# Optimization experiments

Hardware: AMD Instinct MI355X
Metric: run time of the kernel (lower is better)

## Reference

```python
import jax, jax.numpy as jnp
import numpy as np
import math

B, H, W, C = 8, 32, 32, 512
NUM_HEAD_CHANNELS = 64
NUM_HEADS = C // NUM_HEAD_CHANNELS  # 8
HEAD_DIM = C // NUM_HEADS            # 64
NUM_GROUPS = max(1, C // 16)         # 32
EPS = 1e-6  # flax GroupNorm default epsilon


def setup_inputs() -> dict:
    key = jax.random.key(0)
    ks = jax.random.split(key, 7)
    s = lambda fan: 1.0 / math.sqrt(fan)
    return {
        "x": jax.random.normal(ks[0], (B, H, W, C), jnp.float32),
        "gn_scale": jnp.ones((C,), jnp.float32),
        "gn_bias": jnp.zeros((C,), jnp.float32),
        "w_qkv": jax.random.normal(ks[1], (C, 3 * C), jnp.float32) * s(C),
        "b_qkv": jnp.zeros((3 * C,), jnp.float32),
        "w_out": jax.random.normal(ks[2], (C, C), jnp.float32) * s(C),
        "b_out": jnp.zeros((C,), jnp.float32),
    }


def _group_norm(x, scale, bias):
    # x: (B,H,W,C); normalize per (batch, group) over spatial + in-group channels
    b, h, w, c = x.shape
    xg = x.reshape(b, h * w, NUM_GROUPS, c // NUM_GROUPS)
    mu = jnp.mean(xg, axis=(1, 3), keepdims=True)
    var = jnp.var(xg, axis=(1, 3), keepdims=True)
    xn = (xg - mu) * jax.lax.rsqrt(var + EPS)
    return xn.reshape(b, h, w, c) * scale + bias


def reference(x, gn_scale, gn_bias, w_qkv, b_qkv, w_out, b_out):
    b, h, w, c = x.shape
    seq = h * w
    x_flat = x.reshape(b, seq, c)
    x_norm = _group_norm(x, gn_scale, gn_bias).reshape(b, seq, c)
    qkv = x_norm @ w_qkv + b_qkv                      # (b, seq, 3c)
    q, k, v = jnp.split(qkv, 3, axis=-1)
    scale = 1.0 / math.sqrt(HEAD_DIM)

    def to_heads(t):
        return t.reshape(b, seq, NUM_HEADS, HEAD_DIM).transpose(0, 2, 1, 3)

    q, k, v = to_heads(q), to_heads(k), to_heads(v)
    # NOTE: scale applied to both q and k, matching the original module
    weight = jnp.einsum('bhld,bhsd->bhls', q * scale, k * scale)
    weight = jax.nn.softmax(weight, axis=-1)
    out = jnp.einsum('bhls,bhsd->bhld', weight, v)
    out = out.transpose(0, 2, 1, 3).reshape(b, seq, c)
    out = out @ w_out + b_out
    return (x_flat + out).reshape(b, h, w, c)
```

## Files before the change

### kernel.cpp

```cpp
#include <hip/hip_runtime.h>
#include <hip/hip_bf16.h>

#define SEQ   1024
#define CH    512
#define NHEAD 8
#define HDIM  64
#define BATCH 8

using short8  = __attribute__((ext_vector_type(8))) short;
using short4v = __attribute__((ext_vector_type(4))) short;
using floatx4 = __attribute__((ext_vector_type(4))) float;
using uint4v  = __attribute__((ext_vector_type(4))) unsigned int;

#if __has_builtin(__builtin_amdgcn_exp2f)
#define EXP2F __builtin_amdgcn_exp2f
#else
#define EXP2F exp2f
#endif

__device__ inline unsigned short f2bf(float f) {
  __hip_bfloat16 h = __float2bfloat16(f);
  return __builtin_bit_cast(unsigned short, h);
}

__device__ inline unsigned int cvt_pk_bf16(float lo, float hi) {
  unsigned int r;
  asm("v_cvt_pk_bf16_f32 %0, %1, %2" : "=v"(r) : "v"(lo), "v"(hi));
  return r;
}

__device__ inline void load_lds16(const void* g, void* l) {
  __builtin_amdgcn_global_load_lds(
      (const __attribute__((address_space(1))) unsigned int*)g,
      (__attribute__((address_space(3))) unsigned int*)l, 16, 0, 0);
}

__global__ __launch_bounds__(1024) void prep_kernel(
    const float* __restrict__ wqkv, const float* __restrict__ wout,
    const float* __restrict__ x, const float* __restrict__ gsc,
    const float* __restrict__ gbs,
    unsigned short* __restrict__ wqkvt, unsigned short* __restrict__ woutt,
    unsigned short* __restrict__ xn) {
  __shared__ float SH[16416];
  const int blk = blockIdx.x, tid = threadIdx.x;

  if (blk >= 256) {
    const float* src; unsigned short* dst; int C, bx, by;
    if (blk < 448) { int t = blk - 256; src = wqkv; dst = wqkvt; C = 1536; bx = t % 24; by = t / 24; }
    else           { int t = blk - 448; src = wout; dst = woutt; C = 512;  bx = t & 7;  by = t >> 3; }
    float (*T)[65] = (float(*)[65])SH;
    int tx = tid & 63, ty = tid >> 6;
    for (int j = 0; j < 4; ++j)
      T[ty + j * 16][tx] = src[(size_t)(by * 64 + ty + j * 16) * C + bx * 64 + tx];
    __syncthreads();
    for (int j = 0; j < 4; ++j)
      dst[(size_t)(bx * 64 + ty + j * 16) * 512 + by * 64 + tx] = f2bf(T[tx][ty + j * 16]);
    return;
  }

  const int b = blk >> 5, g = blk & 31;
  const size_t base = (size_t)b * SEQ * CH + g * 16;

  float s = 0.f, sq = 0.f;
  for (int i = 0; i < 4; ++i) {
    int c = (i << 10) + tid;
    int r = c >> 2, c4 = (c & 3) << 2;
    float4 v = *(const float4*)(x + base + (size_t)r * CH + c4);
    *(float4*)&SH[c << 2] = v;
    s  += v.x + v.y + v.z + v.w;
    sq += v.x * v.x + v.y * v.y + v.z * v.z + v.w * v.w;
  }
  for (int off = 1; off < 64; off <<= 1) {
    s  += __shfl_xor(s, off);
    sq += __shfl_xor(sq, off);
  }
  const int wid = tid >> 6, lane = tid & 63;
  if (lane == 0) { SH[16384 + wid] = s; SH[16400 + wid] = sq; }
  __syncthreads();
  float ts = 0.f, tq = 0.f;
  for (int i = 0; i < 16; ++i) { ts += SH[16384 + i]; tq += SH[16400 + i]; }
  const float inv_n = 1.0f / 16384.0f;
  float mean = ts * inv_n;
  float var  = tq * inv_n - mean * mean;
  float rstd = rsqrtf(var + 1e-6f);

  int c4 = (tid & 3) << 2;
  float4 sc = *(const float4*)(gsc + g * 16 + c4);
  float4 bs = *(const float4*)(gbs + g * 16 + c4);
  for (int i = 0; i < 4; ++i) {
    int c = (i << 10) + tid;
    int r = c >> 2;
    float4 v = *(const float4*)&SH[c << 2];
    ushort4 o;
    o.x = f2bf((v.x - mean) * rstd * sc.x + bs.x);
    o.y = f2bf((v.y - mean) * rstd * sc.y + bs.y);
    o.z = f2bf((v.z - mean) * rstd * sc.z + bs.z);
    o.w = f2bf((v.w - mean) * rstd * sc.w + bs.w);
    *(ushort4*)(xn + base + (size_t)r * CH + c4) = o;
  }
}

template <int EPI, int MTILE>
__global__ __launch_bounds__(256) void gemm_bt_kernel(
    const unsigned short* __restrict__ A, const unsigned short* __restrict__ Bt,
    int K, int N,
    const float* __restrict__ bias, const float* __restrict__ resid,
    float* __restrict__ outf,
    unsigned short* __restrict__ qb, unsigned short* __restrict__ kb,
    unsigned short* __restrict__ vtb) {
  constexpr int SMSZ = (MTILE == 128) ? 17408 : 16896;
  constexpr int NI   = (MTILE == 128) ? 4 : 2;
  __shared__ alignas(16) unsigned short SM[SMSZ];
  unsigned short* LA = SM;
  unsigned short* LB = SM + MTILE * 64;

  const int tid = threadIdx.x;
  const int wid = tid >> 6, lane = tid & 63;
  const int quad = lane >> 4, m16 = lane & 15;
  const int sw = m16 & 7;
  const int wm = (MTILE == 128) ? (wid & 1) * 64 : 0;
  const int wn = (MTILE == 128) ? (wid >> 1) * 64 : wid * 32;
  const int m0 = blockIdx.x * MTILE, n0 = blockIdx.y * 128;

  floatx4 acc[4][NI];
  for (int i = 0; i < 4; ++i)
    for (int j = 0; j < NI; ++j) acc[i][j] = 0.f;

  for (int k0 = 0; k0 < K; k0 += 64) {
    for (int i = 0; i < MTILE / 32; ++i) {
      int c = i * 256 + tid;
      int r = c >> 3, kc = c & 7;
      load_lds16(A + (size_t)(m0 + r) * K + k0 + ((kc ^ (r & 7)) << 3), &LA[c << 3]);
    }
    for (int i = 0; i < 4; ++i) {
      int c = i * 256 + tid;
      int r = c >> 3, kc = c & 7;
      load_lds16(Bt + (size_t)(n0 + r) * K + k0 + ((kc ^ (r & 7)) << 3), &LB[c << 3]);
    }
    __syncthreads();
    for (int kq = 0; kq < 2; ++kq) {
      int csw = (((kq << 2) + quad) ^ sw) << 3;
      short8 af[4], bf[NI];
      for (int mi = 0; mi < 4; ++mi)
        af[mi] = *(const short8*)&LA[(wm + mi * 16 + m16) * 64 + csw];
      for (int ni = 0; ni < NI; ++ni)
        bf[ni] = *(const short8*)&LB[(wn + ni * 16 + m16) * 64 + csw];
      for (int mi = 0; mi < 4; ++mi)
        for (int ni = 0; ni < NI; ++ni)
          acc[mi][ni] = __builtin_amdgcn_mfma_f32_16x16x32_bf16(af[mi], bf[ni], acc[mi][ni], 0, 0, 0);
    }
    __syncthreads();
  }

  const int b = m0 >> 10;
  if (EPI == 0) {
    const int part = n0 >> 9;
    if (part < 2) {
      const float qscale = (part == 0) ? 0.0225421381f : 1.0f;
      unsigned short* dst = (part == 0) ? qb : kb;
      for (int mi = 0; mi < 4; ++mi)
        for (int ni = 0; ni < 4; ++ni) {
          int ln = wn + ni * 16 + m16;
          float bb = bias[n0 + ln];
          for (int reg = 0; reg < 4; ++reg)
            SM[(wm + mi * 16 + quad * 4 + reg) * 136 + ln] =
                f2bf((acc[mi][ni][reg] + bb) * qscale);
        }
      __syncthreads();
      const int colb = n0 & 511;
      for (int j = 0; j < 8; ++j) {
        int c = j * 256 + tid;
        int m = c >> 4, n8 = (c & 15) * 8;
        int h = (colb + n8) >> 6, d = n8 & 63;
        int sp = (m0 & 1023) + m;
        int4 v = *(const int4*)&SM[m * 136 + n8];
        *(int4*)(dst + (((size_t)(b * NHEAD + h)) * SEQ + sp) * HDIM + d) = v;
      }
    } else {
      for (int mi = 0; mi < 4; ++mi)
        for (int ni = 0; ni < 4; ++ni) {
          int ln = wn + ni * 16 + m16;
          float bb = bias[n0 + ln];
          int mblk = (wm >> 4) + mi;
          int sbase = 32 * (mblk >> 1) + 8 * quad + 4 * (mblk & 1);
          for (int reg = 0; reg < 4; ++reg)
            SM[ln * 136 + sbase + reg] = f2bf(acc[mi][ni][reg] + bb);
        }
      __syncthreads();
      int hbase = (n0 - 1024) >> 6;
      for (int j = 0; j < 8; ++j) {
        int c = j * 256 + tid;
        int ld = c >> 4, sp8 = (c & 15) * 8;
        int h = hbase + (ld >> 6), d = ld & 63;
        int4 v = *(const int4*)&SM[ld * 136 + sp8];
        *(int4*)(vtb + ((size_t)(b * NHEAD + h) * HDIM + d) * SEQ + (m0 & 1023) + sp8) = v;
      }
    }
  } else {
    float* SMf = (float*)SM;
    for (int mi = 0; mi < 4; ++mi)
      for (int ni = 0; ni < NI; ++ni) {
        int ln = wn + ni * 16 + m16;
        float bb = bias[n0 + ln];
        for (int reg = 0; reg < 4; ++reg)
          SMf[(mi * 16 + quad * 4 + reg) * 132 + ln] = acc[mi][ni][reg] + bb;
      }
    __syncthreads();
    for (int j = 0; j < 8; ++j) {
      int c = j * 256 + tid;
      int m = c >> 5, n4 = (c & 31) * 4;
      size_t idx = (size_t)(m0 + m) * N + n0 + n4;
      float4 v = *(const float4*)&SMf[m * 132 + n4];
      float4 rr = *(const float4*)&resid[idx];
      v.x += rr.x; v.y += rr.y; v.z += rr.z; v.w += rr.w;
      *(float4*)&outf[idx] = v;
    }
  }
}

__global__ __launch_bounds__(256) void attn_kernel(
    const unsigned short* __restrict__ qb, const unsigned short* __restrict__ kb,
    const unsigned short* __restrict__ vtb, unsigned short* __restrict__ ao) {
  const int head = blockIdx.x, qt = blockIdx.y;
  const int b = head >> 3, h = head & 7;
  const int tid = threadIdx.x;
  const int wid = tid >> 6, lane = tid & 63;
  const int quad = lane >> 4, m16 = lane & 15;
  const int sw = m16 & 7;

  __shared__ alignas(16) unsigned short sK[2][8192];
  __shared__ alignas(16) unsigned short sV[2][8192];

  const unsigned short* kbase = kb  + (size_t)head * SEQ * HDIM;
  const unsigned short* vbase = vtb + (size_t)head * HDIM * SEQ;

  short8 aq[2][2];
  for (int qblk = 0; qblk < 2; ++qblk) {
    const size_t qrow = (size_t)head * SEQ + qt * 128 + wid * 32 + qblk * 16 + m16;
    aq[qblk][0] = *(const short8*)(qb + qrow * HDIM + quad * 8);
    aq[qblk][1] = *(const short8*)(qb + qrow * HDIM + 32 + quad * 8);
  }

  const unsigned int onep = 0x3F803F80u;
  const short8 vones = __builtin_bit_cast(short8, (uint4v){onep, onep, onep, onep});

  floatx4 la[2];
  floatx4 o[2][4];
  for (int qblk = 0; qblk < 2; ++qblk) {
    la[qblk] = 0.f;
    for (int df = 0; df < 4; ++df) o[qblk][df] = 0.f;
  }

  for (int i = 0; i < 4; ++i) {
    int c = i * 256 + tid;
    int r = c >> 3, kc = c & 7;
    load_lds16(kbase + r * HDIM + ((kc ^ (r & 7)) << 3), &sK[0][c << 3]);
  }
  for (int i = 0; i < 4; ++i) {
    int c = i * 256 + tid;
    int d = c >> 4, kc = c & 15;
    load_lds16(vbase + d * SEQ + ((kc ^ (d & 7)) << 3), &sV[0][c << 3]);
  }
  __syncthreads();

  int buf = 0;
  for (int kt = 0; kt < 8; ++kt) {
    if (kt < 7) {
      const int nb = buf ^ 1, kn = kt + 1;
      for (int i = 0; i < 4; ++i) {
        int c = i * 256 + tid;
        int r = c >> 3, kc = c & 7;
        load_lds16(kbase + (kn * 128 + r) * HDIM + ((kc ^ (r & 7)) << 3), &sK[nb][c << 3]);
      }
      for (int i = 0; i < 4; ++i) {
        int c = i * 256 + tid;
        int d = c >> 4, kc = c & 15;
        load_lds16(vbase + d * SEQ + kn * 128 + ((kc ^ (d & 7)) << 3), &sV[nb][c << 3]);
      }
    }

    unsigned int pw[2][4][4];
    for (int sf = 0; sf < 8; ++sf) {
      const int rb = (sf * 16 + m16) * 64;
      short8 k0 = *(const short8*)&sK[buf][rb + ((quad ^ sw) << 3)];
      short8 k1 = *(const short8*)&sK[buf][rb + (((4 + quad) ^ sw) << 3)];
      floatx4 s0 = 0.f, s1 = 0.f;
      __builtin_amdgcn_s_setprio(1);
      s0 = __builtin_amdgcn_mfma_f32_16x16x32_bf16(k0, aq[0][0], s0, 0, 0, 0);
      s0 = __builtin_amdgcn_mfma_f32_16x16x32_bf16(k1, aq[0][1], s0, 0, 0, 0);
      s1 = __builtin_amdgcn_mfma_f32_16x16x32_bf16(k0, aq[1][0], s1, 0, 0, 0);
      s1 = __builtin_amdgcn_mfma_f32_16x16x32_bf16(k1, aq[1][1], s1, 0, 0, 0);
      __builtin_amdgcn_s_setprio(0);
      const int u = sf >> 1, w2 = (sf & 1) * 2;
      {
        float p0 = EXP2F(s0[0]), p1 = EXP2F(s0[1]);
        float p2 = EXP2F(s0[2]), p3 = EXP2F(s0[3]);
        pw[0][u][w2 + 0] = cvt_pk_bf16(p0, p1);
        pw[0][u][w2 + 1] = cvt_pk_bf16(p2, p3);
      }
      {
        float p0 = EXP2F(s1[0]), p1 = EXP2F(s1[1]);
        float p2 = EXP2F(s1[2]), p3 = EXP2F(s1[3]);
        pw[1][u][w2 + 0] = cvt_pk_bf16(p0, p1);
        pw[1][u][w2 + 1] = cvt_pk_bf16(p2, p3);
      }
    }

    for (int u = 0; u < 4; ++u) {
      const short8 pf0 = __builtin_bit_cast(
          short8, (uint4v){pw[0][u][0], pw[0][u][1], pw[0][u][2], pw[0][u][3]});
      const short8 pf1 = __builtin_bit_cast(
          short8, (uint4v){pw[1][u][0], pw[1][u][1], pw[1][u][2], pw[1][u][3]});
      const int chunk = ((u * 4 + quad) ^ sw) << 3;
      __builtin_amdgcn_s_setprio(1);
      for (int df = 0; df < 4; ++df) {
        short8 bv = *(const short8*)&sV[buf][(df * 16 + m16) * 128 + chunk];
        o[0][df] = __builtin_amdgcn_mfma_f32_16x16x32_bf16(pf0, bv, o[0][df], 0, 0, 0);
        o[1][df] = __builtin_amdgcn_mfma_f32_16x16x32_bf16(pf1, bv, o[1][df], 0, 0, 0);
      }
      la[0] = __builtin_amdgcn_mfma_f32_16x16x32_bf16(pf0, vones, la[0], 0, 0, 0);
      la[1] = __builtin_amdgcn_mfma_f32_16x16x32_bf16(pf1, vones, la[1], 0, 0, 0);
      __builtin_amdgcn_s_setprio(0);
    }
    __syncthreads();
    buf ^= 1;
  }

  for (int qblk = 0; qblk < 2; ++qblk) {
    floatx4 lr;
    for (int r = 0; r < 4; ++r) lr[r] = 1.0f / la[qblk][r];
    int qg = qt * 128 + wid * 32 + qblk * 16 + quad * 4;
    for (int df = 0; df < 4; ++df) {
      int col = h * HDIM + df * 16 + m16;
      size_t base = (size_t)(b * SEQ + qg) * CH + col;
      ao[base + 0 * CH] = f2bf(o[qblk][df][0] * lr[0]);
      ao[base + 1 * CH] = f2bf(o[qblk][df][1] * lr[1]);
      ao[base + 2 * CH] = f2bf(o[qblk][df][2] * lr[2]);
      ao[base + 3 * CH] = f2bf(o[qblk][df][3] * lr[3]);
    }
  }
}

extern "C" void kernel_launch(void* const* d_in, const int* in_sizes, int n_in,
                              void* d_out, int out_size, void* d_ws, size_t ws_size,
                              hipStream_t stream) {
  const float* x    = (const float*)d_in[0];
  const float* gsc  = (const float*)d_in[1];
  const float* gbs  = (const float*)d_in[2];
  const float* wqkv = (const float*)d_in[3];
  const float* bqkv = (const float*)d_in[4];
  const float* wout = (const float*)d_in[5];
  const float* bout = (const float*)d_in[6];
  float* out = (float*)d_out;

  char* ws = (char*)d_ws;
  unsigned short* xn    = (unsigned short*)(ws);
  unsigned short* wqkvt = (unsigned short*)(ws + 8388608);
  unsigned short* woutt = (unsigned short*)(ws + 9961472);
  unsigned short* qb    = (unsigned short*)(ws + 10485760);
  unsigned short* kb    = (unsigned short*)(ws + 18874368);
  unsigned short* vtb   = (unsigned short*)(ws + 27262976);
  unsigned short* ao    = (unsigned short*)(ws + 35651584);

  prep_kernel<<<512, 1024, 0, stream>>>(wqkv, wout, x, gsc, gbs, wqkvt, woutt, xn);
  gemm_bt_kernel<0, 128><<<dim3(64, 12), 256, 0, stream>>>(
      xn, wqkvt, 512, 1536, bqkv, nullptr, nullptr, qb, kb, vtb);
  attn_kernel<<<dim3(64, 8), 256, 0, stream>>>(qb, kb, vtb, ao);
  gemm_bt_kernel<1, 64><<<dim3(128, 4), 256, 0, stream>>>(
      ao, woutt, 512, 512, bout, x, out, nullptr, nullptr, nullptr);
}
```

Measured before the change: 145.4 us.

## Single-buffer attention LDS for occupancy and stage output via LDS for coalesced stores

Drops double-buffered K/V shared memory in the attention kernel in favour of one 32KB buffer, adds a launch-bounds occupancy hint of 4 blocks, and interleaves QK/exp with PV per 32-key chunk so fewer packed probabilities stay live in registers. The output tile is staged through LDS in fp32 and written as 16-byte bf16 vectors instead of scattered 2-byte stores. The aim is more resident waves to hide latency and fewer uncoalesced writes. The cost is that the next K/V tile load no longer overlaps compute inside a block, and an extra sync is added per tile.

```diff
diff --git a/kernel.cpp b/kernel.cpp
--- a/kernel.cpp
+++ b/kernel.cpp
@@ -218,7 +218,7 @@
   }
 }
 
-__global__ __launch_bounds__(256) void attn_kernel(
+__global__ __launch_bounds__(256, 4) void attn_kernel(
     const unsigned short* __restrict__ qb, const unsigned short* __restrict__ kb,
     const unsigned short* __restrict__ vtb, unsigned short* __restrict__ ao) {
   const int head = blockIdx.x, qt = blockIdx.y;
@@ -228,8 +228,9 @@
   const int quad = lane >> 4, m16 = lane & 15;
   const int sw = m16 & 7;
 
-  __shared__ alignas(16) unsigned short sK[2][8192];
-  __shared__ alignas(16) unsigned short sV[2][8192];
+  __shared__ alignas(16) unsigned short SMEM[16384];
+  unsigned short* sK = SMEM;
+  unsigned short* sV = SMEM + 8192;
 
   const unsigned short* kbase = kb  + (size_t)head * SEQ * HDIM;
   const unsigned short* vbase = vtb + (size_t)head * HDIM * SEQ;
@@ -251,70 +252,47 @@
     for (int df = 0; df < 4; ++df) o[qblk][df] = 0.f;
   }
 
-  for (int i = 0; i < 4; ++i) {
-    int c = i * 256 + tid;
-    int r = c >> 3, kc = c & 7;
-    load_lds16(kbase + r * HDIM + ((kc ^ (r & 7)) << 3), &sK[0][c << 3]);
-  }
-  for (int i = 0; i < 4; ++i) {
-    int c = i * 256 + tid;
-    int d = c >> 4, kc = c & 15;
-    load_lds16(vbase + d * SEQ + ((kc ^ (d & 7)) << 3), &sV[0][c << 3]);
-  }
-  __syncthreads();
-
-  int buf = 0;
   for (int kt = 0; kt < 8; ++kt) {
-    if (kt < 7) {
-      const int nb = buf ^ 1, kn = kt + 1;
-      for (int i = 0; i < 4; ++i) {
-        int c = i * 256 + tid;
-        int r = c >> 3, kc = c & 7;
-        load_lds16(kbase + (kn * 128 + r) * HDIM + ((kc ^ (r & 7)) << 3), &sK[nb][c << 3]);
-      }
-      for (int i = 0; i < 4; ++i) {
-        int c = i * 256 + tid;
-        int d = c >> 4, kc = c & 15;
-        load_lds16(vbase + d * SEQ + kn * 128 + ((kc ^ (d & 7)) << 3), &sV[nb][c << 3]);
-      }
-    }
-
-    unsigned int pw[2][4][4];
-    for (int sf = 0; sf < 8; ++sf) {
-      const int rb = (sf * 16 + m16) * 64;
-      short8 k0 = *(const short8*)&sK[buf][rb + ((quad ^ sw) << 3)];
-      short8 k1 = *(const short8*)&sK[buf][rb + (((4 + quad) ^ sw) << 3)];
-      floatx4 s0 = 0.f, s1 = 0.f;
-      __builtin_amdgcn_s_setprio(1);
-      s0 = __builtin_amdgcn_mfma_f32_16x16x32_bf16(k0, aq[0][0], s0, 0, 0, 0);
-      s0 = __builtin_amdgcn_mfma_f32_16x16x32_bf16(k1, aq[0][1], s0, 0, 0, 0);
-      s1 = __builtin_amdgcn_mfma_f32_16x16x32_bf16(k0, aq[1][0], s1, 0, 0, 0);
-      s1 = __builtin_amdgcn_mfma_f32_16x16x32_bf16(k1, aq[1][1], s1, 0, 0, 0);
-      __builtin_amdgcn_s_setprio(0);
-      const int u = sf >> 1, w2 = (sf & 1) * 2;
-      {
-        float p0 = EXP2F(s0[0]), p1 = EXP2F(s0[1]);
-        float p2 = EXP2F(s0[2]), p3 = EXP2F(s0[3]);
-        pw[0][u][w2 + 0] = cvt_pk_bf16(p0, p1);
-        pw[0][u][w2 + 1] = cvt_pk_bf16(p2, p3);
-      }
-      {
-        float p0 = EXP2F(s1[0]), p1 = EXP2F(s1[1]);
-        float p2 = EXP2F(s1[2]), p3 = EXP2F(s1[3]);
-        pw[1][u][w2 + 0] = cvt_pk_bf16(p0, p1);
-        pw[1][u][w2 + 1] = cvt_pk_bf16(p2, p3);
-      }
-    }
+    if (kt) __syncthreads();
+    for (int i = 0; i < 4; ++i) {
+      int c = i * 256 + tid;
+      int r = c >> 3, kc = c & 7;
+      load_lds16(kbase + (kt * 128 + r) * HDIM + ((kc ^ (r & 7)) << 3), &sK[c << 3]);
+    }
+    for (int i = 0; i < 4; ++i) {
+      int c = i * 256 + tid;
+      int d = c >> 4, kc = c & 15;
+      load_lds16(vbase + d * SEQ + kt * 128 + ((kc ^ (d & 7)) << 3), &sV[c << 3]);
+    }
+    __syncthreads();
 
     for (int u = 0; u < 4; ++u) {
+      unsigned int pw[2][4];
+      for (int t = 0; t < 2; ++t) {
+        const int sf = u * 2 + t;
+        const int rb = (sf * 16 + m16) * 64;
+        short8 k0 = *(const short8*)&sK[rb + ((quad ^ sw) << 3)];
+        short8 k1 = *(const short8*)&sK[rb + (((4 + quad) ^ sw) << 3)];
+        floatx4 s0 = 0.f, s1 = 0.f;
+        __builtin_amdgcn_s_setprio(1);
+        s0 = __builtin_amdgcn_mfma_f32_16x16x32_bf16(k0, aq[0][0], s0, 0, 0, 0);
+        s0 = __builtin_amdgcn_mfma_f32_16x16x32_bf16(k1, aq[0][1], s0, 0, 0, 0);
+        s1 = __builtin_amdgcn_mfma_f32_16x16x32_bf16(k0, aq[1][0], s1, 0, 0, 0);
+        s1 = __builtin_amdgcn_mfma_f32_16x16x32_bf16(k1, aq[1][1], s1, 0, 0, 0);
+        __builtin_amdgcn_s_setprio(0);
+        pw[0][t * 2 + 0] = cvt_pk_bf16(EXP2F(s0[0]), EXP2F(s0[1]));
+        pw[0][t * 2 + 1] = cvt_pk_bf16(EXP2F(s0[2]), EXP2F(s0[3]));
+        pw[1][t * 2 + 0] = cvt_pk_bf16(EXP2F(s1[0]), EXP2F(s1[1]));
+        pw[1][t * 2 + 1] = cvt_pk_bf16(EXP2F(s1[2]), EXP2F(s1[3]));
+      }
       const short8 pf0 = __builtin_bit_cast(
-          short8, (uint4v){pw[0][u][0], pw[0][u][1], pw[0][u][2], pw[0][u][3]});
+          short8, (uint4v){pw[0][0], pw[0][1], pw[0][2], pw[0][3]});
       const short8 pf1 = __builtin_bit_cast(
-          short8, (uint4v){pw[1][u][0], pw[1][u][1], pw[1][u][2], pw[1][u][3]});
+          short8, (uint4v){pw[1][0], pw[1][1], pw[1][2], pw[1][3]});
       const int chunk = ((u * 4 + quad) ^ sw) << 3;
       __builtin_amdgcn_s_setprio(1);
       for (int df = 0; df < 4; ++df) {
-        short8 bv = *(const short8*)&sV[buf][(df * 16 + m16) * 128 + chunk];
+        short8 bv = *(const short8*)&sV[(df * 16 + m16) * 128 + chunk];
         o[0][df] = __builtin_amdgcn_mfma_f32_16x16x32_bf16(pf0, bv, o[0][df], 0, 0, 0);
         o[1][df] = __builtin_amdgcn_mfma_f32_16x16x32_bf16(pf1, bv, o[1][df], 0, 0, 0);
       }
@@ -322,22 +300,34 @@
       la[1] = __builtin_amdgcn_mfma_f32_16x16x32_bf16(pf1, vones, la[1], 0, 0, 0);
       __builtin_amdgcn_s_setprio(0);
     }
-    __syncthreads();
-    buf ^= 1;
-  }
-
+  }
+  __syncthreads();
+
+  float* Sc = (float*)SMEM;
   for (int qblk = 0; qblk < 2; ++qblk) {
     floatx4 lr;
     for (int r = 0; r < 4; ++r) lr[r] = 1.0f / la[qblk][r];
-    int qg = qt * 128 + wid * 32 + qblk * 16 + quad * 4;
+    const int row0 = wid * 32 + qblk * 16 + quad * 4;
     for (int df = 0; df < 4; ++df) {
-      int col = h * HDIM + df * 16 + m16;
-      size_t base = (size_t)(b * SEQ + qg) * CH + col;
-      ao[base + 0 * CH] = f2bf(o[qblk][df][0] * lr[0]);
-      ao[base + 1 * CH] = f2bf(o[qblk][df][1] * lr[1]);
-      ao[base + 2 * CH] = f2bf(o[qblk][df][2] * lr[2]);
-      ao[base + 3 * CH] = f2bf(o[qblk][df][3] * lr[3]);
-    }
+      const int col = df * 16 + m16;
+      Sc[(row0 + 0) * 64 + col] = o[qblk][df][0] * lr[0];
+      Sc[(row0 + 1) * 64 + col] = o[qblk][df][1] * lr[1];
+      Sc[(row0 + 2) * 64 + col] = o[qblk][df][2] * lr[2];
+      Sc[(row0 + 3) * 64 + col] = o[qblk][df][3] * lr[3];
+    }
+  }
+  __syncthreads();
+  for (int j = 0; j < 4; ++j) {
+    int c = j * 256 + tid;
+    int m = c >> 3, n8 = (c & 7) * 8;
+    floatx4 v0 = *(const floatx4*)&Sc[m * 64 + n8];
+    floatx4 v1 = *(const floatx4*)&Sc[m * 64 + n8 + 4];
+    int4 w;
+    w.x = (int)cvt_pk_bf16(v0[0], v0[1]);
+    w.y = (int)cvt_pk_bf16(v0[2], v0[3]);
+    w.z = (int)cvt_pk_bf16(v1[0], v1[1]);
+    w.w = (int)cvt_pk_bf16(v1[2], v1[3]);
+    *(int4*)(ao + (size_t)(b * SEQ + qt * 128 + m) * CH + h * HDIM + n8) = w;
   }
 }
 
```

After: 142.4 us. 2.1% less time.
